# Kernel tuning notes

Measured on AMD Instinct MI355X. Metric: run time of the kernel, lower is better.

Reference implementation:

```python
import jax, jax.numpy as jnp
import numpy as np

SEQ, B, IN, H = 512, 64, 1024, 1024

def _lstm_layer(x_seq, Wx, bx, Wh, bh):
    # x_seq: [S, B, D], Wx: [4H, D], Wh: [4H, H]
    h0 = jnp.zeros((x_seq.shape[1], Wh.shape[1]), x_seq.dtype)
    c0 = jnp.zeros_like(h0)
    def step(carry, x_t):
        h, c = carry
        z = x_t @ Wx.T + bx + h @ Wh.T + bh  # [B, 4H]
        i, f, g, o = jnp.split(z, 4, axis=1)
        c1 = jax.nn.sigmoid(f) * c + jax.nn.sigmoid(i) * jnp.tanh(g)
        h1 = jax.nn.sigmoid(o) * jnp.tanh(c1)
        return (h1, c1), h1
    _, hs = jax.lax.scan(step, (h0, c0), x_seq)
    return hs  # [S, B, H]

def setup_inputs() -> dict:
    key = jax.random.key(0)
    ks = jax.random.split(key, 9)
    s_in = 1.0 / np.sqrt(IN)
    s_h = 1.0 / np.sqrt(H)
    return {
        "x": jax.random.normal(ks[0], (SEQ, B, IN), jnp.float32),
        "Wx0": jax.random.uniform(ks[1], (4 * H, IN), jnp.float32, -s_in, s_in),
        "bx0": jax.random.uniform(ks[2], (4 * H,), jnp.float32, -s_in, s_in),
        "Wh0": jax.random.uniform(ks[3], (4 * H, H), jnp.float32, -s_h, s_h),
        "bh0": jax.random.uniform(ks[4], (4 * H,), jnp.float32, -s_h, s_h),
        "Wx1": jax.random.uniform(ks[5], (4 * H, H), jnp.float32, -s_h, s_h),
        "bx1": jax.random.uniform(ks[6], (4 * H,), jnp.float32, -s_h, s_h),
        "Wh1": jax.random.uniform(ks[7], (4 * H, H), jnp.float32, -s_h, s_h),
        "bh1": jax.random.uniform(ks[8], (4 * H,), jnp.float32, -s_h, s_h),
    }

def reference(x, Wx0, bx0, Wh0, bh0, Wx1, bx1, Wh1, bh1):
    # Two stacked unidirectional LSTM layers, zero initial states.
    h_seq0 = _lstm_layer(x, Wx0, bx0, Wh0, bh0)
    h_seq1 = _lstm_layer(h_seq0, Wx1, bx1, Wh1, bh1)
    return h_seq1  # [S, B, H] = stacked version of the torch list output
```

## Files before the change

kernel.cpp:

```cpp
#include <hip/hip_runtime.h>


#define SEQ   512
#define BATCH 64
#define HID   1024
#define NG    4096
#define KCAT  2048
#define EPOCH_IDX 8192

#define SMEM_BYTES 133504

typedef __attribute__((ext_vector_type(8))) _Float16 f16x8;
typedef __attribute__((ext_vector_type(4))) _Float16 f16x4;
typedef __attribute__((ext_vector_type(4))) float    f32x4;

__device__ __forceinline__ float sigm_f(float x){ return 1.f/(1.f + __expf(-x)); }
__device__ __forceinline__ float tanh_f(float x){
    float e = __expf(-2.f*fabsf(x));
    float r = (1.f - e)/(1.f + e);
    return copysignf(r, x);
}

__device__ __forceinline__ void store_h8(_Float16* p, f16x4 v){
    asm volatile("global_store_dwordx2 %0, %1, off sc0 sc1" :: "v"(p), "v"(v) : "memory");
}
__device__ __forceinline__ void drain_vmem(){
    asm volatile("s_waitcnt vmcnt(0)" ::: "memory");
}


__global__ void prep_w_kernel(const float* __restrict__ Wx, const float* __restrict__ Wh,
                              const float* __restrict__ bx, const float* __restrict__ bh,
                              _Float16* __restrict__ Wr, float* __restrict__ br){
    int p = blockIdx.x;
    int j = p >> 2, g = p & 3;
    int r = g*1024 + j;
    int k = threadIdx.x * 8;
    const float* s = (k < 1024) ? (Wx + (size_t)r*1024 + k)
                                : (Wh + (size_t)r*1024 + (k - 1024));
    float4 v0 = *reinterpret_cast<const float4*>(s);
    float4 v1 = *reinterpret_cast<const float4*>(s + 4);
    f16x8 o;
    o[0]=(_Float16)v0.x; o[1]=(_Float16)v0.y; o[2]=(_Float16)v0.z; o[3]=(_Float16)v0.w;
    o[4]=(_Float16)v1.x; o[5]=(_Float16)v1.y; o[6]=(_Float16)v1.z; o[7]=(_Float16)v1.w;
    *reinterpret_cast<f16x8*>(Wr + (size_t)p*KCAT + k) = o;
    if (threadIdx.x == 0) br[p] = bx[r] + bh[r];
}

__global__ void prep_x_kernel(const float* __restrict__ x, _Float16* xo){
    size_t i = ((size_t)blockIdx.x*256 + threadIdx.x) * 8;
    float4 v0 = *reinterpret_cast<const float4*>(x + i);
    float4 v1 = *reinterpret_cast<const float4*>(x + i + 4);
    f16x8 o;
    o[0]=(_Float16)v0.x; o[1]=(_Float16)v0.y; o[2]=(_Float16)v0.z; o[3]=(_Float16)v0.w;
    o[4]=(_Float16)v1.x; o[5]=(_Float16)v1.y; o[6]=(_Float16)v1.z; o[7]=(_Float16)v1.w;
    *reinterpret_cast<f16x8*>(xo + i) = o;
}

__global__ void init_misc_kernel(int* flags, _Float16* hz){
    int i = blockIdx.x*256 + threadIdx.x;
    flags[i] = 0;
    size_t j = (size_t)i * 4;
    if (j < (size_t)BATCH*HID){
        f16x4 z; z[0]=(_Float16)0.f; z[1]=(_Float16)0.f; z[2]=(_Float16)0.f; z[3]=(_Float16)0.f;
        *reinterpret_cast<f16x4*>(hz + j) = z;
    }
}


__device__ __forceinline__ void wait_epoch_g(const int* flags, int k, int rep){
    for(;;){
        int e = __hip_atomic_load(&flags[EPOCH_IDX + rep*32], __ATOMIC_RELAXED, __HIP_MEMORY_SCOPE_AGENT);
        if (e >= k) break;
        __builtin_amdgcn_s_sleep(2);
    }
    asm volatile("" ::: "memory");
}

__device__ __forceinline__ void aggregate_publish(int* flags, int k, int lane){
    const int b = lane*4;
    for(;;){
        int a0 = __hip_atomic_load(&flags[(b+0)*32], __ATOMIC_RELAXED, __HIP_MEMORY_SCOPE_AGENT);
        int a1 = __hip_atomic_load(&flags[(b+1)*32], __ATOMIC_RELAXED, __HIP_MEMORY_SCOPE_AGENT);
        int a2 = __hip_atomic_load(&flags[(b+2)*32], __ATOMIC_RELAXED, __HIP_MEMORY_SCOPE_AGENT);
        int a3 = __hip_atomic_load(&flags[(b+3)*32], __ATOMIC_RELAXED, __HIP_MEMORY_SCOPE_AGENT);
        bool ok = (a0>=k) && (a1>=k) && (a2>=k) && (a3>=k);
        if (__all(ok)) break;
        __builtin_amdgcn_s_sleep(1);
    }
    asm volatile("" ::: "memory");
    if (lane < 8)
        __hip_atomic_store(&flags[EPOCH_IDX + lane*32], k, __ATOMIC_RELAXED, __HIP_MEMORY_SCOPE_AGENT);
}

__device__ __forceinline__ void lds_publish(int* e, int k){
    __hip_atomic_store(e, k, __ATOMIC_RELAXED, __HIP_MEMORY_SCOPE_WORKGROUP);
}
__device__ __forceinline__ void lds_wait(int* e, int k){
    while (__hip_atomic_load(e, __ATOMIC_RELAXED, __HIP_MEMORY_SCOPE_WORKGROUP) < k)
        __builtin_amdgcn_s_sleep(1);
    asm volatile("" ::: "memory");
}


__device__ __forceinline__ f32x4 mfma16(f16x8 a, f16x8 b, f32x4 c){
    return __builtin_amdgcn_mfma_f32_16x16x32_f16(a, b, c, 0, 0, 0);
}

__device__ __forceinline__ void gemm_q_f16(const _Float16* A, const _Float16* Wp, f32x4* acc){
    #pragma unroll 4
    for (int kk = 0; kk < 16; ++kk){
        f16x8 b  = *reinterpret_cast<const f16x8*>(Wp + kk*32);
        f16x8 a0 = *reinterpret_cast<const f16x8*>(A + kk*32);
        f16x8 a1 = *reinterpret_cast<const f16x8*>(A + kk*32 + 16*1024);
        f16x8 a2 = *reinterpret_cast<const f16x8*>(A + kk*32 + 32*1024);
        f16x8 a3 = *reinterpret_cast<const f16x8*>(A + kk*32 + 48*1024);
        acc[0] = mfma16(a0, b, acc[0]);
        acc[1] = mfma16(a1, b, acc[1]);
        acc[2] = mfma16(a2, b, acc[2]);
        acc[3] = mfma16(a3, b, acc[3]);
    }
}

__device__ __forceinline__ void gemm_q_f32(const float* A, const _Float16* Wp, f32x4* acc){
    #pragma unroll 2
    for (int kk = 0; kk < 16; ++kk){
        f16x8 b = *reinterpret_cast<const f16x8*>(Wp + kk*32);
        f16x8 a[4];
        #pragma unroll
        for (int m = 0; m < 4; ++m){
            float4 u0 = *reinterpret_cast<const float4*>(A + kk*32 + (size_t)m*16*1024);
            float4 u1 = *reinterpret_cast<const float4*>(A + kk*32 + (size_t)m*16*1024 + 4);
            f16x8 v;
            v[0]=(_Float16)u0.x; v[1]=(_Float16)u0.y; v[2]=(_Float16)u0.z; v[3]=(_Float16)u0.w;
            v[4]=(_Float16)u1.x; v[5]=(_Float16)u1.y; v[6]=(_Float16)u1.z; v[7]=(_Float16)u1.w;
            a[m] = v;
        }
        acc[0] = mfma16(a[0], b, acc[0]);
        acc[1] = mfma16(a[1], b, acc[1]);
        acc[2] = mfma16(a[2], b, acc[2]);
        acc[3] = mfma16(a[3], b, acc[3]);
    }
}

__device__ __forceinline__ void gemm_q_ldsb(const _Float16* A, const char* wrow,
                                            int c0, int swz, f32x4* acc){
    #pragma unroll 4
    for (int kk = 0; kk < 16; ++kk){
        f16x8 b  = *reinterpret_cast<const f16x8*>(wrow + ((c0 + kk*64) ^ swz));
        f16x8 a0 = *reinterpret_cast<const f16x8*>(A + kk*32);
        f16x8 a1 = *reinterpret_cast<const f16x8*>(A + kk*32 + 16*1024);
        f16x8 a2 = *reinterpret_cast<const f16x8*>(A + kk*32 + 32*1024);
        f16x8 a3 = *reinterpret_cast<const f16x8*>(A + kk*32 + 48*1024);
        acc[0] = mfma16(a0, b, acc[0]);
        acc[1] = mfma16(a1, b, acc[1]);
        acc[2] = mfma16(a2, b, acc[2]);
        acc[3] = mfma16(a3, b, acc[3]);
    }
}


__global__ __launch_bounds__(256, 1)
void lstm_persist(const _Float16* __restrict__ Wr0, const _Float16* __restrict__ Wr1,
                  const float* __restrict__ br0, const float* __restrict__ br1,
                  const _Float16* __restrict__ xbf, const float* __restrict__ xf32,
                  int use_xf16, const _Float16* __restrict__ hz,
                  _Float16* h0ring, _Float16* h1ring, float* out, int* flags){
    extern __shared__ char smem[];
    float (*accL)[4][64][17] = reinterpret_cast<float(*)[4][64][17]>(smem + 98304);
    int* lds_epoch = reinterpret_cast<int*>(smem + 133120);

    const int tid  = threadIdx.x;
    const int wg   = blockIdx.x;
    const int wv   = tid >> 6;
    const int lane = tid & 63;
    const int r    = lane & 15;
    const int q    = lane >> 4;
    const int p0   = wg * 16;
    const int rep  = wg & 7;
    const int swz  = (r & 7) << 4;

    for (int idx = tid; idx < 6144; idx += 256){
        int rr, cb; char* dst; const _Float16* s;
        if (idx < 2048){
            rr = idx >> 7;  cb = (idx & 127) << 4;
            s   = Wr0 + (size_t)(p0 + rr)*KCAT + 1024 + (cb >> 1);
            dst = smem + rr*2048 + (cb ^ ((rr & 7) << 4));
        } else {
            int j2 = idx - 2048;
            rr = j2 >> 8;  cb = (j2 & 255) << 4;
            s   = Wr1 + (size_t)(p0 + rr)*KCAT + (cb >> 1);
            dst = smem + 32768 + rr*4096 + (cb ^ ((rr & 7) << 4));
        }
        *reinterpret_cast<f16x8*>(dst) = *reinterpret_cast<const f16x8*>(s);
    }
    if (tid == 0) *lds_epoch = 0;
    __syncthreads();

    f32x4 cst = {0.f,0.f,0.f,0.f};
    f32x4 ho_keep = {0.f,0.f,0.f,0.f};
    f32x4 bias[4];
    {
        const float* bsrc = (wv == 0) ? br0 : br1;
        #pragma unroll
        for (int jj = 0; jj < 4; ++jj)
            bias[jj] = *reinterpret_cast<const f32x4*>(&bsrc[p0 + jj*4]);
    }

    const int kofs = (wv & 1)*512 + q*8;
    const int wcol = wv*512 + q*8;
    const char* w1row  = smem + 32768 + r*4096;
    const char* wh0row = smem + r*2048;

    for (int k = 0; k <= SEQ; ++k){
        f32x4 acc0[4], acc1[4];
        #pragma unroll
        for (int m = 0; m < 4; ++m){
            acc0[m].x=0;acc0[m].y=0;acc0[m].z=0;acc0[m].w=0;
            acc1[m].x=0;acc1[m].y=0;acc1[m].z=0;acc1[m].w=0;
        }

        if (wv < 2){
            if (k < SEQ){
                if (use_xf16)
                    gemm_q_f16(xbf + (size_t)k*BATCH*HID + (size_t)r*HID + kofs,
                               Wr0 + (size_t)(p0 + r)*KCAT + wcol, acc0);
                else
                    gemm_q_f32(xf32 + (size_t)k*BATCH*1024 + (size_t)r*1024 + kofs,
                               Wr0 + (size_t)(p0 + r)*KCAT + wcol, acc0);
            }
            if (k > 0){
                lds_wait(lds_epoch, k);
                gemm_q_ldsb(h0ring + (size_t)(k-1)*BATCH*HID + (size_t)r*HID + kofs,
                            w1row, wv*1024 + q*16, swz, acc1);
            }
        } else {
            if (k > 0){
                if (wv == 3){
                    if (wg == 0) aggregate_publish(flags, k, lane);
                    else         wait_epoch_g(flags, k, rep);
                    lds_publish(lds_epoch, k);
                } else {
                    lds_wait(lds_epoch, k);
                }
            }
            if (k < SEQ){
                const _Float16* A0 = (k == 0) ? (hz + (size_t)r*HID + kofs)
                                              : (h0ring + (size_t)(k-1)*BATCH*HID + (size_t)r*HID + kofs);
                gemm_q_ldsb(A0, wh0row, (wv-2)*1024 + q*16, swz, acc0);
            }
            if (k >= 1){
                const _Float16* A1 = (k == 1) ? (hz + (size_t)r*HID + kofs)
                                              : (h1ring + (size_t)(k-2)*BATCH*HID + (size_t)r*HID + kofs);
                gemm_q_ldsb(A1, w1row, wv*1024 + q*16, swz, acc1);
            }
        }

        __syncthreads();

        #pragma unroll
        for (int mt = 0; mt < 4; ++mt){
            #pragma unroll
            for (int j = 0; j < 4; ++j){
                accL[0][wv][mt*16 + q*4 + j][r] = acc0[mt][j];
                accL[1][wv][mt*16 + q*4 + j][r] = acc1[mt][j];
            }
        }
        __syncthreads();

        if (wv == 0 && k < SEQ){
            f32x4 zz[4];
            #pragma unroll
            for (int jj = 0; jj < 4; ++jj) zz[jj] = bias[jj];
            #pragma unroll
            for (int w2 = 0; w2 < 4; ++w2)
                #pragma unroll
                for (int jj = 0; jj < 4; ++jj){
                    f32x4 a = *reinterpret_cast<const f32x4*>(&accL[0][w2][lane][jj*4]);
                    zz[jj].x += a.x; zz[jj].y += a.y; zz[jj].z += a.z; zz[jj].w += a.w;
                }
            f16x4 hv;
            #pragma unroll
            for (int jl = 0; jl < 4; ++jl){
                float ig = sigm_f(zz[jl].x), fg = sigm_f(zz[jl].y);
                float gg = tanh_f(zz[jl].z), og = sigm_f(zz[jl].w);
                float c = fg*cst[jl] + ig*gg;  cst[jl] = c;
                hv[jl] = (_Float16)(og * tanh_f(c));
            }
            store_h8(h0ring + ((size_t)k*BATCH + lane)*HID + wg*4, hv);
            drain_vmem();
        }
        if (wv == 1 && k >= 1){
            const int t1 = k - 1;
            f32x4 zz[4];
            #pragma unroll
            for (int jj = 0; jj < 4; ++jj) zz[jj] = bias[jj];
            #pragma unroll
            for (int w2 = 0; w2 < 4; ++w2)
                #pragma unroll
                for (int jj = 0; jj < 4; ++jj){
                    f32x4 a = *reinterpret_cast<const f32x4*>(&accL[1][w2][lane][jj*4]);
                    zz[jj].x += a.x; zz[jj].y += a.y; zz[jj].z += a.z; zz[jj].w += a.w;
                }
            f16x4 hv; f32x4 ho;
            #pragma unroll
            for (int jl = 0; jl < 4; ++jl){
                float ig = sigm_f(zz[jl].x), fg = sigm_f(zz[jl].y);
                float gg = tanh_f(zz[jl].z), og = sigm_f(zz[jl].w);
                float c = fg*cst[jl] + ig*gg;  cst[jl] = c;
                float h = og * tanh_f(c);
                hv[jl] = (_Float16)h;  ho[jl] = h;
            }
            if (k < SEQ) store_h8(h1ring + ((size_t)t1*BATCH + lane)*HID + wg*4, hv);
            if (t1 < SEQ-1) *reinterpret_cast<f32x4*>(out + ((size_t)t1*BATCH + lane)*HID + wg*4) = ho;
            else            ho_keep = ho;
            drain_vmem();
        }

        __syncthreads();
        if (tid == 0)
            __hip_atomic_store(&flags[wg*32], k + 1, __ATOMIC_RELAXED, __HIP_MEMORY_SCOPE_AGENT);
    }

    if (wv == 3){
        if (wg == 0) aggregate_publish(flags, SEQ + 1, lane);
        else         wait_epoch_g(flags, SEQ + 1, rep);
        lds_publish(lds_epoch, SEQ + 1);
    }
    if (wv == 1){
        lds_wait(lds_epoch, SEQ + 1);
        *reinterpret_cast<f32x4*>(out + ((size_t)(SEQ-1)*BATCH + lane)*HID + wg*4) = ho_keep;
    }
}


extern "C" void kernel_launch(void* const* d_in, const int* in_sizes, int n_in,
                              void* d_out, int out_size, void* d_ws, size_t ws_size,
                              hipStream_t stream){
    const float* x   = (const float*)d_in[0];
    const float* Wx0 = (const float*)d_in[1];
    const float* bx0 = (const float*)d_in[2];
    const float* Wh0 = (const float*)d_in[3];
    const float* bh0 = (const float*)d_in[4];
    const float* Wx1 = (const float*)d_in[5];
    const float* bx1 = (const float*)d_in[6];
    const float* Wh1 = (const float*)d_in[7];
    const float* bh1 = (const float*)d_in[8];
    float* out = (float*)d_out;
    char* ws = (char*)d_ws;

    size_t o = 0;
    _Float16* Wr0 = (_Float16*)(ws + o); o += (size_t)NG*KCAT*2;
    _Float16* Wr1 = (_Float16*)(ws + o); o += (size_t)NG*KCAT*2;
    float* br0 = (float*)(ws + o); o += 16384;
    float* br1 = (float*)(ws + o); o += 16384;
    _Float16* h1ring = (_Float16*)(ws + o); o += (size_t)SEQ*BATCH*HID*2;
    _Float16* hz     = (_Float16*)(ws + o); o += (size_t)BATCH*HID*2;
    int* flags = (int*)(ws + o); o += 65536;

    const size_t RING = (size_t)SEQ*BATCH*HID*2;
    _Float16 *xbf = nullptr, *h0ring;
    int use_xf16 = 0;
    if (ws_size >= o + 2*RING){
        xbf    = (_Float16*)(ws + o);  o += RING;  use_xf16 = 1;
        h0ring = (_Float16*)(ws + o);  o += RING;
    } else if (ws_size >= o + RING){
        xbf    = (_Float16*)(ws + o);  o += RING;  use_xf16 = 1;
        h0ring = (_Float16*)((char*)d_out + (size_t)64*1024*1024);
    } else {
        h0ring = (_Float16*)((char*)d_out + (size_t)64*1024*1024);
    }

    hipFuncSetAttribute((const void*)lstm_persist,
                        hipFuncAttributeMaxDynamicSharedMemorySize, SMEM_BYTES);

    prep_w_kernel<<<NG, 256, 0, stream>>>(Wx0, Wh0, bx0, bh0, Wr0, br0);
    prep_w_kernel<<<NG, 256, 0, stream>>>(Wx1, Wh1, bx1, bh1, Wr1, br1);
    if (use_xf16)
        prep_x_kernel<<<(SEQ*BATCH*HID)/(256*8), 256, 0, stream>>>(x, xbf);
    init_misc_kernel<<<64, 256, 0, stream>>>(flags, hz);
    lstm_persist<<<256, 256, SMEM_BYTES, stream>>>(Wr0, Wr1, br0, br1, xbf, x, use_xf16,
                                                   hz, h0ring, h1ring, out, flags);
}
```

Baseline: 9.838 ms.

## Split per-layer grid barriers and software-pipeline A-operand loads in GEMMs

Replaces the single per-step grid barrier with separate flag/epoch sets for layer 0 and layer 1. Layer-0 completion is published right after the layer-0 cell update, so the layer-1 GEMM (and the next step's layer-0 work) can proceed without waiting for a combined barrier. Each timestep now runs as two phases (layer 0 then layer 1), each with its own LDS reduction and __syncthreads. The GEMM helpers are rewritten to double-buffer A-operand loads across k-blocks to hide global latency. The cost is more registers, an extra intra-block sync per step, and more complex cross-block ordering, which risks added latency or subtle races.

Measured after the change: 8.843 ms. 1.11x faster.

```diff
diff --git a/kernel.cpp b/kernel.cpp
--- a/kernel.cpp
+++ b/kernel.cpp
@@ -6,7 +6,10 @@
 #define HID   1024
 #define NG    4096
 #define KCAT  2048
-#define EPOCH_IDX 8192
+#define F0_BASE 0
+#define E0_IDX  8192
+#define F1_BASE 16384
+#define E1_IDX  24576
 
 #define SMEM_BYTES 133504
 
@@ -60,37 +63,37 @@
 __global__ void init_misc_kernel(int* flags, _Float16* hz){
     int i = blockIdx.x*256 + threadIdx.x;
     flags[i] = 0;
-    size_t j = (size_t)i * 4;
-    if (j < (size_t)BATCH*HID){
+    if (i < 16384){
         f16x4 z; z[0]=(_Float16)0.f; z[1]=(_Float16)0.f; z[2]=(_Float16)0.f; z[3]=(_Float16)0.f;
-        *reinterpret_cast<f16x4*>(hz + j) = z;
-    }
-}
-
-
-__device__ __forceinline__ void wait_epoch_g(const int* flags, int k, int rep){
+        *reinterpret_cast<f16x4*>(hz + (size_t)i*4) = z;
+    }
+}
+
+
+__device__ __forceinline__ void wait_epoch_g(const int* flags, int eidx, int k, int rep){
     for(;;){
-        int e = __hip_atomic_load(&flags[EPOCH_IDX + rep*32], __ATOMIC_RELAXED, __HIP_MEMORY_SCOPE_AGENT);
+        int e = __hip_atomic_load(&flags[eidx + rep*32], __ATOMIC_RELAXED, __HIP_MEMORY_SCOPE_AGENT);
         if (e >= k) break;
         __builtin_amdgcn_s_sleep(2);
     }
     asm volatile("" ::: "memory");
 }
 
-__device__ __forceinline__ void aggregate_publish(int* flags, int k, int lane){
+__device__ __forceinline__ void aggregate_publish(int* flags, int base, int eidx,
+                                                  int k, int lane){
     const int b = lane*4;
     for(;;){
-        int a0 = __hip_atomic_load(&flags[(b+0)*32], __ATOMIC_RELAXED, __HIP_MEMORY_SCOPE_AGENT);
-        int a1 = __hip_atomic_load(&flags[(b+1)*32], __ATOMIC_RELAXED, __HIP_MEMORY_SCOPE_AGENT);
-        int a2 = __hip_atomic_load(&flags[(b+2)*32], __ATOMIC_RELAXED, __HIP_MEMORY_SCOPE_AGENT);
-        int a3 = __hip_atomic_load(&flags[(b+3)*32], __ATOMIC_RELAXED, __HIP_MEMORY_SCOPE_AGENT);
+        int a0 = __hip_atomic_load(&flags[base + (b+0)*32], __ATOMIC_RELAXED, __HIP_MEMORY_SCOPE_AGENT);
+        int a1 = __hip_atomic_load(&flags[base + (b+1)*32], __ATOMIC_RELAXED, __HIP_MEMORY_SCOPE_AGENT);
+        int a2 = __hip_atomic_load(&flags[base + (b+2)*32], __ATOMIC_RELAXED, __HIP_MEMORY_SCOPE_AGENT);
+        int a3 = __hip_atomic_load(&flags[base + (b+3)*32], __ATOMIC_RELAXED, __HIP_MEMORY_SCOPE_AGENT);
         bool ok = (a0>=k) && (a1>=k) && (a2>=k) && (a3>=k);
         if (__all(ok)) break;
         __builtin_amdgcn_s_sleep(1);
     }
     asm volatile("" ::: "memory");
     if (lane < 8)
-        __hip_atomic_store(&flags[EPOCH_IDX + lane*32], k, __ATOMIC_RELAXED, __HIP_MEMORY_SCOPE_AGENT);
+        __hip_atomic_store(&flags[eidx + lane*32], k, __ATOMIC_RELAXED, __HIP_MEMORY_SCOPE_AGENT);
 }
 
 __device__ __forceinline__ void lds_publish(int* e, int k){
@@ -107,18 +110,63 @@
     return __builtin_amdgcn_mfma_f32_16x16x32_f16(a, b, c, 0, 0, 0);
 }
 
-__device__ __forceinline__ void gemm_q_f16(const _Float16* A, const _Float16* Wp, f32x4* acc){
-    #pragma unroll 4
-    for (int kk = 0; kk < 16; ++kk){
-        f16x8 b  = *reinterpret_cast<const f16x8*>(Wp + kk*32);
-        f16x8 a0 = *reinterpret_cast<const f16x8*>(A + kk*32);
-        f16x8 a1 = *reinterpret_cast<const f16x8*>(A + kk*32 + 16*1024);
-        f16x8 a2 = *reinterpret_cast<const f16x8*>(A + kk*32 + 32*1024);
-        f16x8 a3 = *reinterpret_cast<const f16x8*>(A + kk*32 + 48*1024);
-        acc[0] = mfma16(a0, b, acc[0]);
-        acc[1] = mfma16(a1, b, acc[1]);
-        acc[2] = mfma16(a2, b, acc[2]);
-        acc[3] = mfma16(a3, b, acc[3]);
+__device__ __forceinline__ void gemm_pipe_ldsb(const _Float16* A, const char* wrow,
+                                               int c0, int swz, f32x4* acc){
+    f16x8 abuf[2][16];
+    #pragma unroll
+    for (int kk = 0; kk < 4; ++kk)
+        #pragma unroll
+        for (int m = 0; m < 4; ++m)
+            abuf[0][kk*4+m] = *reinterpret_cast<const f16x8*>(A + kk*32 + m*16*1024);
+    #pragma unroll
+    for (int b = 0; b < 4; ++b){
+        if (b < 3){
+            #pragma unroll
+            for (int kk = 0; kk < 4; ++kk)
+                #pragma unroll
+                for (int m = 0; m < 4; ++m)
+                    abuf[(b+1)&1][kk*4+m] =
+                        *reinterpret_cast<const f16x8*>(A + (b+1)*128 + kk*32 + m*16*1024);
+        }
+        #pragma unroll
+        for (int kk = 0; kk < 4; ++kk){
+            const int kg = b*4 + kk;
+            f16x8 bb = *reinterpret_cast<const f16x8*>(wrow + ((c0 + kg*64) ^ swz));
+            acc[0] = mfma16(abuf[b&1][kk*4+0], bb, acc[0]);
+            acc[1] = mfma16(abuf[b&1][kk*4+1], bb, acc[1]);
+            acc[2] = mfma16(abuf[b&1][kk*4+2], bb, acc[2]);
+            acc[3] = mfma16(abuf[b&1][kk*4+3], bb, acc[3]);
+        }
+    }
+}
+
+__device__ __forceinline__ void gemm_pipe_gb(const _Float16* A, const _Float16* Wp,
+                                             f32x4* acc){
+    f16x8 abuf[2][16];
+    #pragma unroll
+    for (int kk = 0; kk < 4; ++kk)
+        #pragma unroll
+        for (int m = 0; m < 4; ++m)
+            abuf[0][kk*4+m] = *reinterpret_cast<const f16x8*>(A + kk*32 + m*16*1024);
+    #pragma unroll
+    for (int b = 0; b < 4; ++b){
+        if (b < 3){
+            #pragma unroll
+            for (int kk = 0; kk < 4; ++kk)
+                #pragma unroll
+                for (int m = 0; m < 4; ++m)
+                    abuf[(b+1)&1][kk*4+m] =
+                        *reinterpret_cast<const f16x8*>(A + (b+1)*128 + kk*32 + m*16*1024);
+        }
+        #pragma unroll
+        for (int kk = 0; kk < 4; ++kk){
+            const int kg = b*4 + kk;
+            f16x8 bb = *reinterpret_cast<const f16x8*>(Wp + kg*32);
+            acc[0] = mfma16(abuf[b&1][kk*4+0], bb, acc[0]);
+            acc[1] = mfma16(abuf[b&1][kk*4+1], bb, acc[1]);
+            acc[2] = mfma16(abuf[b&1][kk*4+2], bb, acc[2]);
+            acc[3] = mfma16(abuf[b&1][kk*4+3], bb, acc[3]);
+        }
     }
 }
 
@@ -140,22 +188,6 @@
         acc[1] = mfma16(a[1], b, acc[1]);
         acc[2] = mfma16(a[2], b, acc[2]);
         acc[3] = mfma16(a[3], b, acc[3]);
-    }
-}
-
-__device__ __forceinline__ void gemm_q_ldsb(const _Float16* A, const char* wrow,
-                                            int c0, int swz, f32x4* acc){
-    #pragma unroll 4
-    for (int kk = 0; kk < 16; ++kk){
-        f16x8 b  = *reinterpret_cast<const f16x8*>(wrow + ((c0 + kk*64) ^ swz));
-        f16x8 a0 = *reinterpret_cast<const f16x8*>(A + kk*32);
-        f16x8 a1 = *reinterpret_cast<const f16x8*>(A + kk*32 + 16*1024);
-        f16x8 a2 = *reinterpret_cast<const f16x8*>(A + kk*32 + 32*1024);
-        f16x8 a3 = *reinterpret_cast<const f16x8*>(A + kk*32 + 48*1024);
-        acc[0] = mfma16(a0, b, acc[0]);
-        acc[1] = mfma16(a1, b, acc[1]);
-        acc[2] = mfma16(a2, b, acc[2]);
-        acc[3] = mfma16(a3, b, acc[3]);
     }
 }
 
@@ -168,7 +200,7 @@
                   _Float16* h0ring, _Float16* h1ring, float* out, int* flags){
     extern __shared__ char smem[];
     float (*accL)[4][64][17] = reinterpret_cast<float(*)[4][64][17]>(smem + 98304);
-    int* lds_epoch = reinterpret_cast<int*>(smem + 133120);
+    int* ldsE = reinterpret_cast<int*>(smem + 133120);
 
     const int tid  = threadIdx.x;
     const int wg   = blockIdx.x;
@@ -194,7 +226,7 @@
         }
         *reinterpret_cast<f16x8*>(dst) = *reinterpret_cast<const f16x8*>(s);
     }
-    if (tid == 0) *lds_epoch = 0;
+    if (tid == 0) *ldsE = 0;
     __syncthreads();
 
     f32x4 cst = {0.f,0.f,0.f,0.f};
@@ -211,61 +243,44 @@
     const int wcol = wv*512 + q*8;
     const char* w1row  = smem + 32768 + r*4096;
     const char* wh0row = smem + r*2048;
+    const size_t BH = (size_t)BATCH*HID;
 
     for (int k = 0; k <= SEQ; ++k){
-        f32x4 acc0[4], acc1[4];
-        #pragma unroll
-        for (int m = 0; m < 4; ++m){
-            acc0[m].x=0;acc0[m].y=0;acc0[m].z=0;acc0[m].w=0;
-            acc1[m].x=0;acc1[m].y=0;acc1[m].z=0;acc1[m].w=0;
-        }
+        f32x4 acc[4];
+        #pragma unroll
+        for (int m = 0; m < 4; ++m){ acc[m].x=0;acc[m].y=0;acc[m].z=0;acc[m].w=0; }
 
         if (wv < 2){
             if (k < SEQ){
                 if (use_xf16)
-                    gemm_q_f16(xbf + (size_t)k*BATCH*HID + (size_t)r*HID + kofs,
-                               Wr0 + (size_t)(p0 + r)*KCAT + wcol, acc0);
+                    gemm_pipe_gb(xbf + (size_t)k*BH + (size_t)r*HID + kofs,
+                                 Wr0 + (size_t)(p0 + r)*KCAT + wcol, acc);
                 else
-                    gemm_q_f32(xf32 + (size_t)k*BATCH*1024 + (size_t)r*1024 + kofs,
-                               Wr0 + (size_t)(p0 + r)*KCAT + wcol, acc0);
-            }
-            if (k > 0){
-                lds_wait(lds_epoch, k);
-                gemm_q_ldsb(h0ring + (size_t)(k-1)*BATCH*HID + (size_t)r*HID + kofs,
-                            w1row, wv*1024 + q*16, swz, acc1);
+                    gemm_q_f32(xf32 + (size_t)k*BH + (size_t)r*HID + kofs,
+                               Wr0 + (size_t)(p0 + r)*KCAT + wcol, acc);
             }
         } else {
             if (k > 0){
                 if (wv == 3){
-                    if (wg == 0) aggregate_publish(flags, k, lane);
-                    else         wait_epoch_g(flags, k, rep);
-                    lds_publish(lds_epoch, k);
+                    if (wg == 0) aggregate_publish(flags, F0_BASE, E0_IDX, k, lane);
+                    else         wait_epoch_g(flags, E0_IDX, k, rep);
+                    lds_publish(ldsE, k);
                 } else {
-                    lds_wait(lds_epoch, k);
+                    lds_wait(ldsE, k);
                 }
             }
             if (k < SEQ){
                 const _Float16* A0 = (k == 0) ? (hz + (size_t)r*HID + kofs)
-                                              : (h0ring + (size_t)(k-1)*BATCH*HID + (size_t)r*HID + kofs);
-                gemm_q_ldsb(A0, wh0row, (wv-2)*1024 + q*16, swz, acc0);
-            }
-            if (k >= 1){
-                const _Float16* A1 = (k == 1) ? (hz + (size_t)r*HID + kofs)
-                                              : (h1ring + (size_t)(k-2)*BATCH*HID + (size_t)r*HID + kofs);
-                gemm_q_ldsb(A1, w1row, wv*1024 + q*16, swz, acc1);
-            }
-        }
-
-        __syncthreads();
-
-        #pragma unroll
-        for (int mt = 0; mt < 4; ++mt){
-            #pragma unroll
-            for (int j = 0; j < 4; ++j){
-                accL[0][wv][mt*16 + q*4 + j][r] = acc0[mt][j];
-                accL[1][wv][mt*16 + q*4 + j][r] = acc1[mt][j];
-            }
-        }
+                                              : (h0ring + (size_t)(k-1)*BH + (size_t)r*HID + kofs);
+                gemm_pipe_ldsb(A0, wh0row, (wv-2)*1024 + q*16, swz, acc);
+            }
+        }
+
+        #pragma unroll
+        for (int mt = 0; mt < 4; ++mt)
+            #pragma unroll
+            for (int j = 0; j < 4; ++j)
+                accL[0][wv][mt*16 + q*4 + j][r] = acc[mt][j];
         __syncthreads();
 
         if (wv == 0 && k < SEQ){
@@ -289,7 +304,36 @@
             }
             store_h8(h0ring + ((size_t)k*BATCH + lane)*HID + wg*4, hv);
             drain_vmem();
-        }
+            if (lane == 0)
+                __hip_atomic_store(&flags[F0_BASE + wg*32], k + 1,
+                                   __ATOMIC_RELAXED, __HIP_MEMORY_SCOPE_AGENT);
+        }
+
+        #pragma unroll
+        for (int m = 0; m < 4; ++m){ acc[m].x=0;acc[m].y=0;acc[m].z=0;acc[m].w=0; }
+
+        if (k >= 1){
+            if (wv < 2){
+                gemm_pipe_ldsb(h0ring + (size_t)(k-1)*BH + (size_t)r*HID + kofs,
+                               w1row, wv*1024 + q*16, swz, acc);
+            } else {
+                if (k >= 2){
+                    if (wg == 0 && wv == 2) aggregate_publish(flags, F1_BASE, E1_IDX, k-1, lane);
+                    else                    wait_epoch_g(flags, E1_IDX, k-1, rep);
+                }
+                const _Float16* A1 = (k == 1) ? (hz + (size_t)r*HID + kofs)
+                                              : (h1ring + (size_t)(k-2)*BH + (size_t)r*HID + kofs);
+                gemm_pipe_ldsb(A1, w1row, wv*1024 + q*16, swz, acc);
+            }
+        }
+
+        #pragma unroll
+        for (int mt = 0; mt < 4; ++mt)
+            #pragma unroll
+            for (int j = 0; j < 4; ++j)
+                accL[1][wv][mt*16 + q*4 + j][r] = acc[mt][j];
+        __syncthreads();
+
         if (wv == 1 && k >= 1){
             const int t1 = k - 1;
             f32x4 zz[4];
@@ -315,20 +359,18 @@
             if (t1 < SEQ-1) *reinterpret_cast<f32x4*>(out + ((size_t)t1*BATCH + lane)*HID + wg*4) = ho;
             else            ho_keep = ho;
             drain_vmem();
-        }
-
-        __syncthreads();
-        if (tid == 0)
-            __hip_atomic_store(&flags[wg*32], k + 1, __ATOMIC_RELAXED, __HIP_MEMORY_SCOPE_AGENT);
-    }
-
-    if (wv == 3){
-        if (wg == 0) aggregate_publish(flags, SEQ + 1, lane);
-        else         wait_epoch_g(flags, SEQ + 1, rep);
-        lds_publish(lds_epoch, SEQ + 1);
-    }
+            if (lane == 0)
+                __hip_atomic_store(&flags[F1_BASE + wg*32], k,
+                                   __ATOMIC_RELAXED, __HIP_MEMORY_SCOPE_AGENT);
+        }
+    }
+
+    if (tid == 0)
+        __hip_atomic_store(&flags[F0_BASE + wg*32], SEQ + 1,
+                           __ATOMIC_RELAXED, __HIP_MEMORY_SCOPE_AGENT);
+    if (wg == 0 && wv == 3) aggregate_publish(flags, F0_BASE, E0_IDX, SEQ + 1, lane);
     if (wv == 1){
-        lds_wait(lds_epoch, SEQ + 1);
+        wait_epoch_g(flags, E0_IDX, SEQ + 1, rep);
         *reinterpret_cast<f32x4*>(out + ((size_t)(SEQ-1)*BATCH + lane)*HID + wg*4) = ho_keep;
     }
 }
@@ -356,7 +398,7 @@
     float* br1 = (float*)(ws + o); o += 16384;
     _Float16* h1ring = (_Float16*)(ws + o); o += (size_t)SEQ*BATCH*HID*2;
     _Float16* hz     = (_Float16*)(ws + o); o += (size_t)BATCH*HID*2;
-    int* flags = (int*)(ws + o); o += 65536;
+    int* flags = (int*)(ws + o); o += 131072;
 
     const size_t RING = (size_t)SEQ*BATCH*HID*2;
     _Float16 *xbf = nullptr, *h0ring;
@@ -378,7 +420,7 @@
     prep_w_kernel<<<NG, 256, 0, stream>>>(Wx1, Wh1, bx1, bh1, Wr1, br1);
     if (use_xf16)
         prep_x_kernel<<<(SEQ*BATCH*HID)/(256*8), 256, 0, stream>>>(x, xbf);
-    init_misc_kernel<<<64, 256, 0, stream>>>(flags, hz);
+    init_misc_kernel<<<128, 256, 0, stream>>>(flags, hz);
     lstm_persist<<<256, 256, SMEM_BYTES, stream>>>(Wr0, Wr1, br0, br1, xbf, x, use_xf16,
                                                    hz, h0ring, h1ring, out, flags);
 }
```
